# Performance work log

Measured on AMD Instinct MI355X. Metric: run time of the kernel, lower is better.

The kernel has to match this reference:

```python
import jax, jax.numpy as jnp
import numpy as np

N = 2048          # num nodes
E = 65536         # num edges
EDGE_DIM = 64
L = 5             # max_path_distance
D_NODE = 128


def setup_inputs() -> dict:
    key = jax.random.key(0)
    k1, k2, k3, k4, k5 = jax.random.split(key, 5)
    x = jax.random.normal(k1, (N, D_NODE), dtype=jnp.float32)
    edge_attr = jax.random.normal(k2, (E, EDGE_DIM), dtype=jnp.float32)
    edge_vector = jax.random.normal(k3, (L, EDGE_DIM), dtype=jnp.float32)  # learned param
    edge_paths_length = jax.random.randint(k4, (N, N), 0, L + 1, dtype=jnp.int64)
    idx = jax.random.randint(k5, (N, N, L), 0, E, dtype=jnp.int64)
    # positions beyond the path length are padded with -1, matching the
    # convention the torch module expects (mask = edge_paths_tensor != -1)
    pos = jnp.arange(L, dtype=jnp.int64)
    edge_paths_tensor = jnp.where(pos[None, None, :] < edge_paths_length[:, :, None], idx, -1)
    return {
        "x": x,
        "edge_attr": edge_attr,
        "edge_vector": edge_vector,
        "edge_paths_tensor": edge_paths_tensor,
        "edge_paths_length": edge_paths_length,
    }


def reference(x, edge_attr, edge_vector, edge_paths_tensor, edge_paths_length):
    # Per-edge, per-position dot products: dots[e, l] = edge_attr[e] . edge_vector[l]
    # This is mathematically identical to gathering [N,N,L,edge_dim] then dotting,
    # but avoids materializing the huge intermediate.
    dots = jnp.einsum("ed,ld->el", edge_attr, edge_vector)  # [E, L]

    mask = edge_paths_tensor != -1                      # [N, N, L]
    safe_idx = jnp.where(mask, edge_paths_tensor, 0)    # [N, N, L]
    pos = jnp.arange(edge_vector.shape[0])              # [L]
    gathered = dots[safe_idx, pos[None, None, :]]       # [N, N, L]

    dp_sum = jnp.sum(gathered * mask, axis=-1)          # [N, N]

    len_f = edge_paths_length.astype(dp_sum.dtype)
    valid = edge_paths_length > 0
    cij = jnp.where(valid, dp_sum / (len_f + 1e-10), jnp.zeros_like(dp_sum))
    return jnp.nan_to_num(cij)
```

## Files before the change

### kernel.cpp

```cpp
#include <hip/hip_runtime.h>

#define NN   2048
#define EE   65536
#define EDIM 64
#define LL   5
#define TPK2 262144

__global__ __launch_bounds__(256) void dots_kernel(
    const float* __restrict__ edge_attr,
    const float* __restrict__ edge_vector,
    _Float16* __restrict__ dotsT) {
  const int lane = threadIdx.x & 63;
  const int wib  = threadIdx.x >> 6;
  const int dg   = lane & 15;
  const int es   = lane >> 4;
  const int e    = blockIdx.x * 16 + wib * 4 + es;

  const float4 a = *(const float4*)(edge_attr + e * EDIM + dg * 4);
  float d[LL];
#pragma unroll
  for (int l = 0; l < LL; ++l) {
    const float4 ev = *(const float4*)(edge_vector + l * EDIM + dg * 4);
    d[l] = a.x * ev.x + a.y * ev.y + a.z * ev.z + a.w * ev.w;
  }
#pragma unroll
  for (int s = 1; s <= 8; s <<= 1) {
#pragma unroll
    for (int l = 0; l < LL; ++l) d[l] += __shfl_xor(d[l], s, 64);
  }
  if (dg < LL) {
    const float dv = (dg == 0) ? d[0] : (dg == 1) ? d[1] : (dg == 2) ? d[2]
                   : (dg == 3) ? d[3] : d[4];
    dotsT[dg * EE + e] = (_Float16)dv;
  }
}

__global__ __launch_bounds__(1024, 4) void pairs_kernel(
    const int* __restrict__ ept,
    const _Float16* __restrict__ dotsT,
    float* __restrict__ out) {
  __shared__ __align__(16) unsigned short tab[EE + 8];
  const int tid = blockIdx.x * 1024 + threadIdx.x;

  int adr[80];
  unsigned cp0 = 0u, cp1 = 0u;
#pragma unroll
  for (int g = 0; g < 4; ++g) {
    const size_t gid = (size_t)g * TPK2 + (size_t)tid;
    const int4* p = (const int4*)(ept + gid * 20);
#pragma unroll
    for (int q = 0; q < 5; ++q) {
      const int4 v = p[q];
#pragma unroll
      for (int jj = 0; jj < 4; ++jj) {
        const int si = q * 4 + jj;
        const int k  = g * 4 + si / 5;
        const int id = (jj == 0) ? v.x : (jj == 1) ? v.y : (jj == 2) ? v.z : v.w;
        adr[g * 20 + si] = (id < 0) ? (EE * 2) : (id * 2);
        const unsigned m = (id >= 0) ? 1u : 0u;
        if (k < 8) cp0 += m << ((k & 7) * 4); else cp1 += m << ((k & 7) * 4);
      }
    }
  }

  float sum[16];
#pragma unroll
  for (int k = 0; k < 16; ++k) sum[k] = 0.f;

  const char* tabb = (const char*)tab;
  if (threadIdx.x == 0) tab[EE] = 0;

#pragma unroll
  for (int l = 0; l < LL; ++l) {
    __syncthreads();
    const float4* src = (const float4*)(dotsT + (size_t)l * EE);
    float4* dst = (float4*)tab;
#pragma unroll
    for (int r = 0; r < 8; ++r)
      dst[r * 1024 + threadIdx.x] = src[r * 1024 + threadIdx.x];
    __syncthreads();
#pragma unroll
    for (int k = 0; k < 16; ++k)
      sum[k] += (float)*(const _Float16*)(tabb + adr[k * 5 + l]);
  }

#pragma unroll
  for (int g = 0; g < 4; ++g) {
    const size_t gid = (size_t)g * TPK2 + (size_t)tid;
    float rr[4];
#pragma unroll
    for (int j = 0; j < 4; ++j) {
      const int k = g * 4 + j;
      const unsigned cnt = (((k < 8) ? cp0 : cp1) >> ((k & 7) * 4)) & 15u;
      rr[j] = sum[k] / ((float)cnt + 1e-10f);
    }
    ((float4*)out)[gid] = make_float4(rr[0], rr[1], rr[2], rr[3]);
  }
}

extern "C" void kernel_launch(void* const* d_in, const int* in_sizes, int n_in,
                              void* d_out, int out_size, void* d_ws, size_t ws_size,
                              hipStream_t stream) {
  const float* edge_attr   = (const float*)d_in[1];
  const float* edge_vector = (const float*)d_in[2];
  const int*   ept         = (const int*)d_in[3];
  float* out = (float*)d_out;
  _Float16* dotsT = (_Float16*)d_ws;

  dots_kernel<<<EE / 16, 256, 0, stream>>>(edge_attr, edge_vector, dotsT);

  pairs_kernel<<<256, 1024, 0, stream>>>(ept, dotsT, out);
}
```

Before: 41.67 us.

## Pre-transpose edge paths to 16-bit per-position indices before gather

Adds a transpose kernel that packs path indices into 16-bit values laid out per path position, plus per-pair counts. The gather kernel then streams compact indices for each position instead of holding 80 addresses in registers. Padded entries map to index 0 and a suffix-sum correction of table[0] values is subtracted at the end, which removes the extra table sentinel. The cost is an extra kernel launch and a full extra pass that reads the int32 edge-path tensor and writes about 50 MB of intermediates, kept only if the workspace is large enough.

```diff
diff --git a/kernel.cpp b/kernel.cpp
--- a/kernel.cpp
+++ b/kernel.cpp
@@ -5,6 +5,7 @@
 #define EDIM 64
 #define LL   5
 #define TPK2 262144
+#define NP   ((size_t)NN * NN)
 
 __global__ __launch_bounds__(256) void dots_kernel(
     const float* __restrict__ edge_attr,
@@ -35,7 +36,111 @@
   }
 }
 
-__global__ __launch_bounds__(1024, 4) void pairs_kernel(
+__global__ __launch_bounds__(256) void transpose_kernel(
+    const int* __restrict__ ept,
+    unsigned short* __restrict__ adrT,
+    unsigned* __restrict__ cnts) {
+  const int t = blockIdx.x * 256 + threadIdx.x;
+  const int4* p = (const int4*)(ept + (size_t)t * 20);
+  int raw[20];
+#pragma unroll
+  for (int q = 0; q < 5; ++q) {
+    const int4 v = p[q];
+    raw[q * 4 + 0] = v.x; raw[q * 4 + 1] = v.y;
+    raw[q * 4 + 2] = v.z; raw[q * 4 + 3] = v.w;
+  }
+  unsigned cw = 0u;
+  unsigned a[20];
+#pragma unroll
+  for (int j = 0; j < 4; ++j) {
+#pragma unroll
+    for (int l = 0; l < LL; ++l) {
+      const int id = raw[j * 5 + l];
+      a[l * 4 + j] = (id < 0) ? 0u : (unsigned)id;
+      cw += ((id >= 0) ? 1u : 0u) << (j * 4);
+    }
+  }
+#pragma unroll
+  for (int l = 0; l < LL; ++l) {
+    uint2 w;
+    w.x = a[l * 4 + 0] | (a[l * 4 + 1] << 16);
+    w.y = a[l * 4 + 2] | (a[l * 4 + 3] << 16);
+    ((uint2*)(adrT + (size_t)l * NP))[t] = w;
+  }
+  cnts[t] = cw;
+}
+
+__global__ __launch_bounds__(1024) void gather_kernel(
+    const unsigned short* __restrict__ adrT,
+    const unsigned* __restrict__ cnts,
+    const _Float16* __restrict__ dotsT,
+    float* __restrict__ out) {
+  __shared__ __align__(16) unsigned short tab[EE];
+  const int tid = blockIdx.x * 1024 + threadIdx.x;
+
+  const unsigned w0 = cnts[0 * TPK2 + tid];
+  const unsigned w1 = cnts[1 * TPK2 + tid];
+  const unsigned w2 = cnts[2 * TPK2 + tid];
+  const unsigned w3 = cnts[3 * TPK2 + tid];
+  const unsigned cp0 = w0 | (w1 << 16);
+  const unsigned cp1 = w2 | (w3 << 16);
+
+  float sum[16];
+#pragma unroll
+  for (int k = 0; k < 16; ++k) sum[k] = 0.f;
+  float t0v[LL];
+
+  const char* tabb = (const char*)tab;
+
+#pragma unroll
+  for (int l = 0; l < LL; ++l) {
+    __syncthreads();
+    const float4* src = (const float4*)(dotsT + (size_t)l * EE);
+    float4* dst = (float4*)tab;
+#pragma unroll
+    for (int r = 0; r < 8; ++r)
+      dst[r * 1024 + threadIdx.x] = src[r * 1024 + threadIdx.x];
+    __syncthreads();
+    t0v[l] = (float)*(const _Float16*)tabb;
+    const uint2* ap = (const uint2*)(adrT + (size_t)l * NP);
+#pragma unroll
+    for (int g = 0; g < 4; ++g) {
+      const uint2 a = ap[g * TPK2 + tid];
+      const unsigned e0 = a.x & 0xffffu, e1 = a.x >> 16;
+      const unsigned e2 = a.y & 0xffffu, e3 = a.y >> 16;
+      sum[g * 4 + 0] += (float)*(const _Float16*)(tabb + 2 * e0);
+      sum[g * 4 + 1] += (float)*(const _Float16*)(tabb + 2 * e1);
+      sum[g * 4 + 2] += (float)*(const _Float16*)(tabb + 2 * e2);
+      sum[g * 4 + 3] += (float)*(const _Float16*)(tabb + 2 * e3);
+    }
+  }
+
+  const float S4 = t0v[4];
+  const float S3 = S4 + t0v[3];
+  const float S2 = S3 + t0v[2];
+  const float S1 = S2 + t0v[1];
+  const float S0 = S1 + t0v[0];
+
+#pragma unroll
+  for (int g = 0; g < 4; ++g) {
+    const size_t gid = (size_t)g * TPK2 + (size_t)tid;
+    float rr[4];
+#pragma unroll
+    for (int j = 0; j < 4; ++j) {
+      const int k = g * 4 + j;
+      const unsigned cnt = (((k < 8) ? cp0 : cp1) >> ((k & 7) * 4)) & 15u;
+      const float corr = (cnt == 5) ? 0.f
+                       : (cnt == 4) ? S4
+                       : (cnt == 3) ? S3
+                       : (cnt == 2) ? S2
+                       : (cnt == 1) ? S1 : S0;
+      rr[j] = (sum[k] - corr) / ((float)cnt + 1e-10f);
+    }
+    ((float4*)out)[gid] = make_float4(rr[0], rr[1], rr[2], rr[3]);
+  }
+}
+
+__global__ __launch_bounds__(1024) void pairs_fallback(
     const int* __restrict__ ept,
     const _Float16* __restrict__ dotsT,
     float* __restrict__ out) {
@@ -62,14 +167,11 @@
       }
     }
   }
-
   float sum[16];
 #pragma unroll
   for (int k = 0; k < 16; ++k) sum[k] = 0.f;
-
   const char* tabb = (const char*)tab;
   if (threadIdx.x == 0) tab[EE] = 0;
-
 #pragma unroll
   for (int l = 0; l < LL; ++l) {
     __syncthreads();
@@ -83,7 +185,6 @@
     for (int k = 0; k < 16; ++k)
       sum[k] += (float)*(const _Float16*)(tabb + adr[k * 5 + l]);
   }
-
 #pragma unroll
   for (int g = 0; g < 4; ++g) {
     const size_t gid = (size_t)g * TPK2 + (size_t)tid;
@@ -105,9 +206,21 @@
   const float* edge_vector = (const float*)d_in[2];
   const int*   ept         = (const int*)d_in[3];
   float* out = (float*)d_out;
-  _Float16* dotsT = (_Float16*)d_ws;
+
+  const size_t dots_bytes = (size_t)LL * EE * 2;
+  const size_t adr_bytes  = (size_t)LL * NP * 2;
+  const size_t cnt_bytes  = NP;
+
+  _Float16* dotsT      = (_Float16*)d_ws;
+  unsigned short* adrT = (unsigned short*)((char*)d_ws + dots_bytes);
+  unsigned* cnts       = (unsigned*)((char*)d_ws + dots_bytes + adr_bytes);
 
   dots_kernel<<<EE / 16, 256, 0, stream>>>(edge_attr, edge_vector, dotsT);
 
-  pairs_kernel<<<256, 1024, 0, stream>>>(ept, dotsT, out);
-}
+  if (ws_size >= dots_bytes + adr_bytes + cnt_bytes) {
+    transpose_kernel<<<(int)(NP / 4 / 256), 256, 0, stream>>>(ept, adrT, cnts);
+    gather_kernel<<<256, 1024, 0, stream>>>(adrT, cnts, dotsT, out);
+  } else {
+    pairs_fallback<<<256, 1024, 0, stream>>>(ept, dotsT, out);
+  }
+}
```

After: 53.30 us. 1.28x slower.
